# Kernel optimization log

Hardware: AMD Instinct MI355X
Metric: run time of the kernel (lower is better)

Reference implementation:

```python
import jax, jax.numpy as jnp
import numpy as np

RATIO = 4

def positional_encoding(d_model, max_len, w_s):
    # w_s: (B,) per-example frequency warp. pe[b, p, 0::2]=sin, pe[b, p, 1::2]=cos
    pos = jnp.arange(max_len, dtype=jnp.float32)                      # (L,)
    div = jnp.power(10000.0, jnp.arange(0, d_model, 2, dtype=jnp.float32) / d_model)  # (d/2,)
    ang = w_s[:, None, None] * pos[None, :, None] / div[None, None, :]  # (B, L, d/2)
    pe = jnp.stack([jnp.sin(ang), jnp.cos(ang)], axis=-1)             # (B, L, d/2, 2)
    return pe.reshape(w_s.shape[0], max_len, d_model)

def setup_inputs() -> dict:
    key = jax.random.key(0)
    ks = jax.random.split(key, 6)
    B, Tds, L, D = 32, 2048, 512, 256
    q = jax.random.normal(ks[0], (B, Tds, D), dtype=jnp.float32)
    k = jax.random.normal(ks[1], (B, L, D), dtype=jnp.float32)
    v = jax.random.normal(ks[2], (B, L, D), dtype=jnp.float32)
    w_compress = jax.random.normal(ks[3], (D // RATIO, D), dtype=jnp.float32) * (D ** -0.5)
    text_lengths = jax.random.randint(ks[4], (B,), L // 2, L + 1).at[0].set(L)
    mel_lengths = jax.random.randint(ks[5], (B,), (Tds * RATIO) // 2, Tds * RATIO + 1).at[0].set(Tds * RATIO)
    return {"q": q, "k": k, "v": v, "w_compress": w_compress,
            "text_lengths": text_lengths, "mel_lengths": mel_lengths}

def reference(q, k, v, w_compress, text_lengths, mel_lengths):
    B, Tds, D = q.shape
    L = k.shape[1]
    # padding masks (True = padded)
    text_mask = jnp.arange(L)[None, :] >= text_lengths[:, None]            # (B, L)
    mel_mask_ds = jnp.arange(Tds)[None, :] >= (mel_lengths // RATIO)[:, None]  # (B, Tds)
    # positional encodings
    q = q + positional_encoding(D, Tds, jnp.ones((B,), dtype=jnp.float32))
    w_s = mel_lengths.astype(jnp.float32) / RATIO / text_lengths.astype(jnp.float32)
    k = k + positional_encoding(D, L, w_s)
    q = q * (float(D) ** -0.5)
    # scores + masked softmax over text axis
    scores = jnp.einsum('btd,bld->btl', q, k)                              # (B, Tds, L)
    scores = jnp.where(text_mask[:, None, :], -jnp.inf, scores)
    align = jax.nn.softmax(scores, axis=-1)
    align = jnp.where(mel_mask_ds[:, :, None], 0.0, align)
    # hard argmax one-hot, straight-through blend
    idx = jnp.argmax(align, axis=-1)                                       # (B, Tds)
    align_oh = jax.nn.one_hot(idx, L, dtype=align.dtype)
    align_oh = jnp.where(mel_mask_ds[:, :, None], 0.0, align_oh)
    blend = align + jax.lax.stop_gradient(align_oh - align)
    attn = jnp.einsum('btl,bld->btd', blend, v)                            # (B, Tds, D)
    # Compress (Linear D -> D//ratio, no bias) then transpose(1,2)
    out = jnp.einsum('btd,cd->bct', attn, w_compress)                      # (B, D//ratio, Tds)
    return out, align
```

## Files before the change

### kernel.cpp

```cpp
#include <hip/hip_runtime.h>
#include <math.h>

#define NB  32
#define TDS 2048
#define LL  512
#define DD  256
#define DC  64
#define GAP_THR 4e-4f

typedef __attribute__((ext_vector_type(8)))  short short8;
typedef __attribute__((ext_vector_type(16))) float f32x16;

__device__ __forceinline__ unsigned short f2bf(float x) {
    union { float f; unsigned u; } v; v.f = x;
    unsigned r = v.u + 0x7fffu + ((v.u >> 16) & 1u);
    return (unsigned short)(r >> 16);
}
__device__ __forceinline__ float bf2f(unsigned short h) {
    union { unsigned u; float f; } v; v.u = ((unsigned)h) << 16;
    return v.f;
}
__device__ __forceinline__ void rr_sincosf(double ang, float* s, float* c) {
    double n = rint(ang * 0.15915494309189535);
    double red = fma(n, -6.283185307179586, ang);
    sincosf((float)red, s, c);
}


__global__ __launch_bounds__(256)
void tables_kernel(const float* __restrict__ k,
                   const int* __restrict__ text_lengths,
                   const int* __restrict__ mel_lengths,
                   float* __restrict__ peq,
                   char* __restrict__ kps,
                   int* __restrict__ cnt) {
    const int tid = threadIdx.x;
    if (blockIdx.x < 2048) {
        int idx = blockIdx.x * 256 + tid;
        if (idx == 0) cnt[0] = 0;
        int t = idx >> 8;
        int d = idx & 255;
        int i = d >> 1;
        double invd = exp((double)i * (-9.210340371976184 / 128.0));
        double ang = (double)t * invd;
        double s, c;
        sincos(ang, &s, &c);
        peq[idx] = (float)((d & 1) ? c : s);
        return;
    }
    __shared__ double invdiv[128];
    if (tid < 128) invdiv[tid] = exp((double)tid * (-9.210340371976184 / 128.0));
    __syncthreads();
    int f = (blockIdx.x - 2048) * 256 + tid;
    int b = f >> 14;
    int r = f & 16383;
    int ks = r >> 11;
    int r2 = r & 2047;
    int cs = r2 >> 7;
    int r3 = r2 & 127;
    int kh = r3 >> 6;
    int g  = (r3 >> 5) & 1;
    int lane32 = r3 & 31;
    int l  = cs * 32 + lane32;
    int k0 = ks * 32 + kh * 16 + g * 8;
    const float* kr = k + ((size_t)(b * LL + l)) * DD + k0;
    float4 kv0 = *(const float4*)(kr);
    float4 kv1 = *(const float4*)(kr + 4);
    float kv[8] = {kv0.x, kv0.y, kv0.z, kv0.w, kv1.x, kv1.y, kv1.z, kv1.w};
    double wsd = ((double)mel_lengths[b] * 0.25) / (double)text_lengths[b];
    double base_ang = wsd * (double)l;
    unsigned short h[8], lo8[8];
#pragma unroll
    for (int jj = 0; jj < 4; ++jj) {
        int i = (k0 >> 1) + jj;
        float sn, cs2;
        rr_sincosf(base_ang * invdiv[i], &sn, &cs2);
        float e0 = kv[2 * jj] + sn;
        float e1 = kv[2 * jj + 1] + cs2;
        h[2 * jj]       = f2bf(e0);
        h[2 * jj + 1]   = f2bf(e1);
        lo8[2 * jj]     = f2bf(e0 - bf2f(h[2 * jj]));
        lo8[2 * jj + 1] = f2bf(e1 - bf2f(h[2 * jj + 1]));
    }
    size_t off = (size_t)b * 524288 + (size_t)ks * 65536 + (size_t)cs * 4096
               + kh * 1024 + g * 512 + lane32 * 16;
    uint4 hv, lv;
    hv.x = h[0] | ((unsigned)h[1] << 16); hv.y = h[2] | ((unsigned)h[3] << 16);
    hv.z = h[4] | ((unsigned)h[5] << 16); hv.w = h[6] | ((unsigned)h[7] << 16);
    lv.x = lo8[0] | ((unsigned)lo8[1] << 16); lv.y = lo8[2] | ((unsigned)lo8[3] << 16);
    lv.z = lo8[4] | ((unsigned)lo8[5] << 16); lv.w = lo8[6] | ((unsigned)lo8[7] << 16);
    *(uint4*)(kps + off) = hv;
    *(uint4*)(kps + off + 2048) = lv;
}

__global__ __launch_bounds__(256, 3)
void score_kernel(const float* __restrict__ q,
                  const float* __restrict__ peq,
                  const char* __restrict__ kps,
                  const int* __restrict__ text_lengths,
                  const int* __restrict__ mel_lengths,
                  float* __restrict__ align_out,
                  int* __restrict__ idx_out,
                  int* __restrict__ flag_cnt,
                  int* __restrict__ flags) {
    __shared__ alignas(16) char smA[32768];
    struct Epi {
        float v1[4][32]; int i1[4][32]; float v2[4][32];
        float S[4][32];  float M[32];
    };
    __shared__ Epi ep;

    const int wgid = blockIdx.x;
    const int xcd = wgid & 7, loc = wgid >> 3;
    const int nid = xcd * 256 + loc;
    const int b  = nid >> 6;
    const int t0 = (nid & 63) << 5;

    const int tid = threadIdx.x;
    const int wn = tid >> 6, lane = tid & 63;
    const int c31 = lane & 31, hi5 = lane >> 5;
    const int tlen = text_lengths[b];
    const int melq = mel_lengths[b] >> 2;

    const char* kpb = kps + (size_t)b * 524288 + (size_t)(hi5 * 512 + c31 * 16);

    f32x16 acc[4];
#pragma unroll
    for (int ci = 0; ci < 4; ++ci)
#pragma unroll
        for (int rg = 0; rg < 16; ++rg) acc[ci][rg] = 0.f;

#define BLOAD(dst, ksv, civ)                                                    \
    {                                                                           \
        const char* p_ = kpb + (ksv) * 65536 + (wn * 4 + (civ)) * 4096;         \
        (dst)[0] = *(const short8*)(p_);                                        \
        (dst)[1] = *(const short8*)(p_ + 1024);                                 \
        (dst)[2] = *(const short8*)(p_ + 2048);                                 \
        (dst)[3] = *(const short8*)(p_ + 3072);                                 \
    }
#define MFMA6(CI, B)                                                            \
    {                                                                           \
        acc[CI] = __builtin_amdgcn_mfma_f32_32x32x16_bf16(ah0, (B)[0], acc[CI], 0, 0, 0); \
        acc[CI] = __builtin_amdgcn_mfma_f32_32x32x16_bf16(ah0, (B)[2], acc[CI], 0, 0, 0); \
        acc[CI] = __builtin_amdgcn_mfma_f32_32x32x16_bf16(al0, (B)[0], acc[CI], 0, 0, 0); \
        acc[CI] = __builtin_amdgcn_mfma_f32_32x32x16_bf16(ah1, (B)[1], acc[CI], 0, 0, 0); \
        acc[CI] = __builtin_amdgcn_mfma_f32_32x32x16_bf16(ah1, (B)[3], acc[CI], 0, 0, 0); \
        acc[CI] = __builtin_amdgcn_mfma_f32_32x32x16_bf16(al1, (B)[1], acc[CI], 0, 0, 0); \
    }

    short8 Bs[3][4];
    BLOAD(Bs[0], 0, 0)
    BLOAD(Bs[1], 0, 1)

    {
        const int sr = tid >> 3, kc = tid & 7;
        const float* qr = q   + ((size_t)(b * TDS) + t0 + sr) * DD;
        const float* pr = peq + (size_t)(t0 + sr) * DD;
#pragma unroll
        for (int kq = 0; kq < 4; ++kq) {
            int m = kq * 8 + kc;
            int k0 = m * 8;
            float4 qa = *(const float4*)(qr + k0);
            float4 qb4 = *(const float4*)(qr + k0 + 4);
            float4 pa = *(const float4*)(pr + k0);
            float4 pb = *(const float4*)(pr + k0 + 4);
            float e[8] = {(qa.x + pa.x) * 0.0625f, (qa.y + pa.y) * 0.0625f,
                          (qa.z + pa.z) * 0.0625f, (qa.w + pa.w) * 0.0625f,
                          (qb4.x + pb.x) * 0.0625f, (qb4.y + pb.y) * 0.0625f,
                          (qb4.z + pb.z) * 0.0625f, (qb4.w + pb.w) * 0.0625f};
            unsigned short h[8], lo[8];
#pragma unroll
            for (int j = 0; j < 8; ++j) {
                h[j] = f2bf(e[j]);
                lo[j] = f2bf(e[j] - bf2f(h[j]));
            }
            uint4 hv, lv;
            hv.x = h[0] | ((unsigned)h[1] << 16); hv.y = h[2] | ((unsigned)h[3] << 16);
            hv.z = h[4] | ((unsigned)h[5] << 16); hv.w = h[6] | ((unsigned)h[7] << 16);
            lv.x = lo[0] | ((unsigned)lo[1] << 16); lv.y = lo[2] | ((unsigned)lo[3] << 16);
            lv.z = lo[4] | ((unsigned)lo[5] << 16); lv.w = lo[6] | ((unsigned)lo[7] << 16);
            int base = (m >> 2) * 4096 + ((m >> 1) & 1) * 1024 + (m & 1) * 512 + sr * 16;
            *(uint4*)(smA + base) = hv;
            *(uint4*)(smA + base + 2048) = lv;
        }
    }
    __syncthreads();

    const int afr = hi5 * 512 + c31 * 16;
    short8 ah0, ah1, al0, al1;
#pragma unroll
    for (int p = 0; p < 32; ++p) {
        if ((p & 3) == 0) {
            const char* ab = smA + (p >> 2) * 4096 + afr;
            ah0 = *(const short8*)(ab);
            ah1 = *(const short8*)(ab + 1024);
            al0 = *(const short8*)(ab + 2048);
            al1 = *(const short8*)(ab + 3072);
        }
        if (p + 2 < 32) BLOAD(Bs[(p + 2) % 3], (p + 2) >> 2, (p + 2) & 3)
        MFMA6(p & 3, Bs[p % 3])
    }
#undef BLOAD
#undef MFMA6

    const float NEGINF = -__builtin_inff();
#pragma unroll
    for (int ci = 0; ci < 4; ++ci) {
        int col = wn * 128 + ci * 32 + c31;
        if (col >= tlen) {
#pragma unroll
            for (int rg = 0; rg < 16; ++rg) acc[ci][rg] = NEGINF;
        }
    }
    float v1[16]; int i1[16]; float v2[16];
#pragma unroll
    for (int rg = 0; rg < 16; ++rg) {
        v1[rg] = acc[0][rg]; i1[rg] = wn * 128 + c31; v2[rg] = NEGINF;
#pragma unroll
        for (int ci = 1; ci < 4; ++ci) {
            float v = acc[ci][rg]; int col = wn * 128 + ci * 32 + c31;
            if (v > v1[rg]) { v2[rg] = v1[rg]; v1[rg] = v; i1[rg] = col; }
            else if (v > v2[rg]) v2[rg] = v;
        }
    }
#pragma unroll
    for (int off = 1; off <= 16; off <<= 1) {
#pragma unroll
        for (int rg = 0; rg < 16; ++rg) {
            float ov1 = __shfl_xor(v1[rg], off, 64);
            int   oi1 = __shfl_xor(i1[rg], off, 64);
            float ov2 = __shfl_xor(v2[rg], off, 64);
            if (ov1 > v1[rg]) { v2[rg] = fmaxf(v1[rg], ov2); v1[rg] = ov1; i1[rg] = oi1; }
            else if (ov1 < v1[rg]) { v2[rg] = fmaxf(v2[rg], ov1); }
            else { i1[rg] = min(i1[rg], oi1); v2[rg] = v1[rg]; }
        }
    }
    if (c31 == 0) {
#pragma unroll
        for (int rg = 0; rg < 16; ++rg) {
            int r32 = (rg & 3) + 8 * (rg >> 2) + 4 * hi5;
            ep.v1[wn][r32] = v1[rg]; ep.i1[wn][r32] = i1[rg]; ep.v2[wn][r32] = v2[rg];
        }
    }
    __syncthreads();
    {
        const int r32 = c31;
        float V1 = ep.v1[0][r32]; int I1 = ep.i1[0][r32]; float V2 = ep.v2[0][r32];
#pragma unroll
        for (int w = 1; w < 4; ++w) {
            float cv1 = ep.v1[w][r32]; int ci1 = ep.i1[w][r32]; float cv2 = ep.v2[w][r32];
            if (cv1 > V1) { V2 = fmaxf(V1, cv2); V1 = cv1; I1 = ci1; }
            else if (cv1 < V1) { V2 = fmaxf(V2, cv1); }
            else { V2 = V1; }
        }
        if (wn == 0 && hi5 == 0) {
            int t = t0 + r32;
            idx_out[b * TDS + t] = I1;
            if (t < melq && (V1 - V2) < GAP_THR) {
                int pos = atomicAdd(flag_cnt, 1);
                flags[pos] = (b << 11) | t;
            }
            ep.M[r32] = V1;
        }
    }
    __syncthreads();
    float ssum[16];
#pragma unroll
    for (int rg = 0; rg < 16; ++rg) {
        int r32 = (rg & 3) + 8 * (rg >> 2) + 4 * hi5;
        float M = ep.M[r32];
        float s = 0.f;
#pragma unroll
        for (int ci = 0; ci < 4; ++ci) {
            float p = __expf(acc[ci][rg] - M);
            acc[ci][rg] = p; s += p;
        }
        ssum[rg] = s;
    }
#pragma unroll
    for (int off = 1; off <= 16; off <<= 1)
#pragma unroll
        for (int rg = 0; rg < 16; ++rg) ssum[rg] += __shfl_xor(ssum[rg], off, 64);
    if (c31 == 0) {
#pragma unroll
        for (int rg = 0; rg < 16; ++rg) {
            int r32 = (rg & 3) + 8 * (rg >> 2) + 4 * hi5;
            ep.S[wn][r32] = ssum[rg];
        }
    }
    __syncthreads();
#pragma unroll
    for (int rg = 0; rg < 16; ++rg) {
        int r32 = (rg & 3) + 8 * (rg >> 2) + 4 * hi5;
        int t = t0 + r32;
        float denom = ep.S[0][r32] + ep.S[1][r32] + ep.S[2][r32] + ep.S[3][r32];
        float sc = (t < melq) ? (1.0f / denom) : 0.f;
        size_t obase = ((size_t)(b * TDS + t)) * LL + wn * 128 + c31;
#pragma unroll
        for (int ci = 0; ci < 4; ++ci)
            __builtin_nontemporal_store(acc[ci][rg] * sc, align_out + obase + ci * 32);
    }
}

__global__ __launch_bounds__(256)
void refine_kernel(const float* __restrict__ q,
                   const float* __restrict__ k,
                   const int* __restrict__ text_lengths,
                   const int* __restrict__ mel_lengths,
                   const int* __restrict__ flags,
                   const int* __restrict__ flag_cnt,
                   int* __restrict__ idx_out) {
    __shared__ double qd[DD];
    __shared__ double invdiv[128];
    __shared__ double rbest[4];
    __shared__ int    ribest[4];
    const int tid = threadIdx.x;
    if (tid < 128)
        invdiv[tid] = 1.0 / pow(10000.0, (double)tid * (1.0 / 128.0));
    const int cnt = flag_cnt[0];
    for (int r = blockIdx.x; r < cnt; r += gridDim.x) {
        const int code = flags[r];
        const int b = code >> 11, t = code & 2047;
        const int tlen = text_lengths[b];
        const double ws = ((double)mel_lengths[b] * 0.25) / (double)text_lengths[b];
        __syncthreads();
        {
            const int d = tid, i = d >> 1;
            float sn, cs;
            rr_sincosf((double)t * invdiv[i], &sn, &cs);
            qd[d] = ((double)q[((size_t)b * TDS + t) * DD + d]
                     + (double)((d & 1) ? cs : sn)) * 0.0625;
        }
        __syncthreads();
        double best = -1.0e300; int bi = 0x7fffffff;
        for (int p = 0; p < 2; ++p) {
            const int l = tid + p * 256;
            if (l < tlen) {
                const float* kr = k + ((size_t)b * LL + l) * DD;
                const double wl = ws * (double)l;
                double sacc = 0.0;
                for (int i = 0; i < 128; ++i) {
                    float sn, cs;
                    rr_sincosf(wl * invdiv[i], &sn, &cs);
                    sacc += ((double)kr[2 * i]     + (double)sn) * qd[2 * i];
                    sacc += ((double)kr[2 * i + 1] + (double)cs) * qd[2 * i + 1];
                }
                if (sacc > best || (sacc == best && l < bi)) { best = sacc; bi = l; }
            }
        }
        for (int off = 1; off <= 32; off <<= 1) {
            double ov = __shfl_xor(best, off, 64);
            int   oi = __shfl_xor(bi, off, 64);
            if (ov > best || (ov == best && oi < bi)) { best = ov; bi = oi; }
        }
        const int wv = tid >> 6;
        if ((tid & 63) == 0) { rbest[wv] = best; ribest[wv] = bi; }
        __syncthreads();
        if (tid == 0) {
            double bb = rbest[0]; int ii = ribest[0];
            for (int w = 1; w < 4; ++w)
                if (rbest[w] > bb || (rbest[w] == bb && ribest[w] < ii)) { bb = rbest[w]; ii = ribest[w]; }
            idx_out[b * TDS + t] = ii;
        }
    }
}

__global__ __launch_bounds__(256)
void compress_kernel(const float* __restrict__ v,
                     const float* __restrict__ wc,
                     const int* __restrict__ idx_in,
                     const int* __restrict__ mel_lengths,
                     float* __restrict__ out) {
    __shared__ float Ws[16 * 68];
    __shared__ float Vs[16 * 68];
    __shared__ int   idxs[64];
    const int b   = blockIdx.y;
    const int t0  = blockIdx.x * 64;
    const int tid = threadIdx.x;
    const int melq = mel_lengths[b] >> 2;
    const float* vb = v + (size_t)b * LL * DD;

    if (tid < 64) {
        int t = t0 + tid;
        int ii = idx_in[b * TDS + t];
        idxs[tid] = (t >= melq) ? -1 : ii;
    }

    const int tx = tid >> 5;
    const int ty = tid & 31;
    const int sc = tid >> 2;
    const int su = tid & 3;
    float acc[8][2];
#pragma unroll
    for (int i = 0; i < 8; ++i) { acc[i][0] = 0.f; acc[i][1] = 0.f; }

    for (int ks = 0; ks < 16; ++ks) {
        const int d0 = ks * 16;
        __syncthreads();
        {
            float4 wv = *(const float4*)(wc + (size_t)sc * DD + d0 + su * 4);
            Ws[(su * 4 + 0) * 68 + sc] = wv.x;
            Ws[(su * 4 + 1) * 68 + sc] = wv.y;
            Ws[(su * 4 + 2) * 68 + sc] = wv.z;
            Ws[(su * 4 + 3) * 68 + sc] = wv.w;
            int row = idxs[sc];
            float4 vv = make_float4(0.f, 0.f, 0.f, 0.f);
            if (row >= 0) vv = *(const float4*)(vb + (size_t)row * DD + d0 + su * 4);
            Vs[(su * 4 + 0) * 68 + sc] = vv.x;
            Vs[(su * 4 + 1) * 68 + sc] = vv.y;
            Vs[(su * 4 + 2) * 68 + sc] = vv.z;
            Vs[(su * 4 + 3) * 68 + sc] = vv.w;
        }
        __syncthreads();
#pragma unroll
        for (int kk = 0; kk < 16; ++kk) {
            const float* wrow = Ws + kk * 68 + tx * 8;
            float4 a0 = *(const float4*)(wrow);
            float4 a1 = *(const float4*)(wrow + 4);
            float2 bb = *(const float2*)(Vs + kk * 68 + ty * 2);
            const float av[8] = {a0.x, a0.y, a0.z, a0.w, a1.x, a1.y, a1.z, a1.w};
#pragma unroll
            for (int i = 0; i < 8; ++i) {
                acc[i][0] = fmaf(av[i], bb.x, acc[i][0]);
                acc[i][1] = fmaf(av[i], bb.y, acc[i][1]);
            }
        }
    }
#pragma unroll
    for (int i = 0; i < 8; ++i) {
        int c = tx * 8 + i;
        float2 o = make_float2(acc[i][0], acc[i][1]);
        *(float2*)(out + ((size_t)(b * DC + c)) * TDS + t0 + ty * 2) = o;
    }
}

extern "C" void kernel_launch(void* const* d_in, const int* in_sizes, int n_in,
                              void* d_out, int out_size, void* d_ws, size_t ws_size,
                              hipStream_t stream) {
    const float* q    = (const float*)d_in[0];
    const float* k    = (const float*)d_in[1];
    const float* v    = (const float*)d_in[2];
    const float* wc   = (const float*)d_in[3];
    const int*   text = (const int*)d_in[4];
    const int*   mel  = (const int*)d_in[5];

    float* out   = (float*)d_out;
    float* align = out + (size_t)NB * DC * TDS;

    char*  wsb = (char*)d_ws;
    char*  KPS = wsb;
    float* PEQ = (float*)(wsb + 16777216);
    int*   IDX = (int*)(wsb + 16777216 + 2097152);
    int*   CNT = IDX + (size_t)NB * TDS;
    int*   FLG = CNT + 1;

    hipLaunchKernelGGL(tables_kernel, dim3(4096), dim3(256), 0, stream,
                       k, text, mel, PEQ, KPS, CNT);
    hipLaunchKernelGGL(score_kernel, dim3(2048), dim3(256), 0, stream,
                       q, PEQ, KPS, text, mel, align, IDX, CNT, FLG);
    hipLaunchKernelGGL(refine_kernel, dim3(256), dim3(256), 0, stream,
                       q, k, text, mel, FLG, CNT, IDX);
    hipLaunchKernelGGL(compress_kernel, dim3(TDS / 64, NB), dim3(256), 0, stream,
                       v, wc, IDX, mel, out);
}
```

Baseline: 199.5 us.

## Transpose MFMA operands so each lane owns one row, simplifying softmax epilogue

Swaps the A/B operands of the bf16 MFMAs so the accumulator is transposed: each lane now holds a single query row with 16 consecutive-ish text columns. The row-wise max/argmax/second-max and softmax sum become mostly in-register with a single cross-half shuffle, which removes the 5-stage butterfly shuffles and one block barrier. Output stores become 16-byte vector nontemporal stores instead of scalar strided stores. Tie handling in argmax now also takes the min index across waves, and correctness depends on the transposed fragment-to-column mapping being right.

```diff
diff --git a/kernel.cpp b/kernel.cpp
--- a/kernel.cpp
+++ b/kernel.cpp
@@ -10,6 +10,7 @@
 
 typedef __attribute__((ext_vector_type(8)))  short short8;
 typedef __attribute__((ext_vector_type(16))) float f32x16;
+typedef __attribute__((ext_vector_type(4)))  float f32x4;
 
 __device__ __forceinline__ unsigned short f2bf(float x) {
     union { float f; unsigned u; } v; v.f = x;
@@ -105,8 +106,7 @@
                   int* __restrict__ flags) {
     __shared__ alignas(16) char smA[32768];
     struct Epi {
-        float v1[4][32]; int i1[4][32]; float v2[4][32];
-        float S[4][32];  float M[32];
+        float v1[4][32]; int i1[4][32]; float v2[4][32]; float S[4][32];
     };
     __shared__ Epi ep;
 
@@ -140,12 +140,12 @@
     }
 #define MFMA6(CI, B)                                                            \
     {                                                                           \
-        acc[CI] = __builtin_amdgcn_mfma_f32_32x32x16_bf16(ah0, (B)[0], acc[CI], 0, 0, 0); \
-        acc[CI] = __builtin_amdgcn_mfma_f32_32x32x16_bf16(ah0, (B)[2], acc[CI], 0, 0, 0); \
-        acc[CI] = __builtin_amdgcn_mfma_f32_32x32x16_bf16(al0, (B)[0], acc[CI], 0, 0, 0); \
-        acc[CI] = __builtin_amdgcn_mfma_f32_32x32x16_bf16(ah1, (B)[1], acc[CI], 0, 0, 0); \
-        acc[CI] = __builtin_amdgcn_mfma_f32_32x32x16_bf16(ah1, (B)[3], acc[CI], 0, 0, 0); \
-        acc[CI] = __builtin_amdgcn_mfma_f32_32x32x16_bf16(al1, (B)[1], acc[CI], 0, 0, 0); \
+        acc[CI] = __builtin_amdgcn_mfma_f32_32x32x16_bf16((B)[0], ah0, acc[CI], 0, 0, 0); \
+        acc[CI] = __builtin_amdgcn_mfma_f32_32x32x16_bf16((B)[2], ah0, acc[CI], 0, 0, 0); \
+        acc[CI] = __builtin_amdgcn_mfma_f32_32x32x16_bf16((B)[0], al0, acc[CI], 0, 0, 0); \
+        acc[CI] = __builtin_amdgcn_mfma_f32_32x32x16_bf16((B)[1], ah1, acc[CI], 0, 0, 0); \
+        acc[CI] = __builtin_amdgcn_mfma_f32_32x32x16_bf16((B)[3], ah1, acc[CI], 0, 0, 0); \
+        acc[CI] = __builtin_amdgcn_mfma_f32_32x32x16_bf16((B)[1], al1, acc[CI], 0, 0, 0); \
     }
 
     short8 Bs[3][4];
@@ -204,102 +204,69 @@
 #undef MFMA6
 
     const float NEGINF = -__builtin_inff();
+    const int t = t0 + c31;
+
+    float v1 = NEGINF, v2 = NEGINF; int i1 = 0x7fffffff;
 #pragma unroll
     for (int ci = 0; ci < 4; ++ci) {
-        int col = wn * 128 + ci * 32 + c31;
-        if (col >= tlen) {
-#pragma unroll
-            for (int rg = 0; rg < 16; ++rg) acc[ci][rg] = NEGINF;
-        }
-    }
-    float v1[16]; int i1[16]; float v2[16];
-#pragma unroll
-    for (int rg = 0; rg < 16; ++rg) {
-        v1[rg] = acc[0][rg]; i1[rg] = wn * 128 + c31; v2[rg] = NEGINF;
-#pragma unroll
-        for (int ci = 1; ci < 4; ++ci) {
-            float v = acc[ci][rg]; int col = wn * 128 + ci * 32 + c31;
-            if (v > v1[rg]) { v2[rg] = v1[rg]; v1[rg] = v; i1[rg] = col; }
-            else if (v > v2[rg]) v2[rg] = v;
-        }
-    }
-#pragma unroll
-    for (int off = 1; off <= 16; off <<= 1) {
+        const int lbase = wn * 128 + ci * 32 + 4 * hi5;
 #pragma unroll
         for (int rg = 0; rg < 16; ++rg) {
-            float ov1 = __shfl_xor(v1[rg], off, 64);
-            int   oi1 = __shfl_xor(i1[rg], off, 64);
-            float ov2 = __shfl_xor(v2[rg], off, 64);
-            if (ov1 > v1[rg]) { v2[rg] = fmaxf(v1[rg], ov2); v1[rg] = ov1; i1[rg] = oi1; }
-            else if (ov1 < v1[rg]) { v2[rg] = fmaxf(v2[rg], ov1); }
-            else { i1[rg] = min(i1[rg], oi1); v2[rg] = v1[rg]; }
-        }
-    }
-    if (c31 == 0) {
+            int l = lbase + (rg & 3) + 8 * (rg >> 2);
+            float v = acc[ci][rg];
+            if (l >= tlen) { v = NEGINF; acc[ci][rg] = NEGINF; }
+            if (v > v1)      { v2 = v1; v1 = v; i1 = l; }
+            else if (v == v1) { i1 = min(i1, l); v2 = v1; }
+            else if (v > v2) { v2 = v; }
+        }
+    }
+    {
+        float ov1 = __shfl_xor(v1, 32, 64);
+        int   oi1 = __shfl_xor(i1, 32, 64);
+        float ov2 = __shfl_xor(v2, 32, 64);
+        if (ov1 > v1)      { v2 = fmaxf(v1, ov2); v1 = ov1; i1 = oi1; }
+        else if (ov1 < v1) { v2 = fmaxf(v2, ov1); }
+        else               { i1 = min(i1, oi1); v2 = v1; }
+    }
+    if (hi5 == 0) { ep.v1[wn][c31] = v1; ep.i1[wn][c31] = i1; ep.v2[wn][c31] = v2; }
+    __syncthreads();
+    float V1 = ep.v1[0][c31]; int I1 = ep.i1[0][c31]; float V2 = ep.v2[0][c31];
+#pragma unroll
+    for (int w = 1; w < 4; ++w) {
+        float cv1 = ep.v1[w][c31]; int ci1 = ep.i1[w][c31]; float cv2 = ep.v2[w][c31];
+        if (cv1 > V1)      { V2 = fmaxf(V1, cv2); V1 = cv1; I1 = ci1; }
+        else if (cv1 < V1) { V2 = fmaxf(V2, cv1); }
+        else               { I1 = min(I1, ci1); V2 = V1; }
+    }
+    if (tid < 32) {
+        idx_out[b * TDS + t] = I1;
+        if (t < melq && (V1 - V2) < GAP_THR) {
+            int pos = atomicAdd(flag_cnt, 1);
+            flags[pos] = (b << 11) | t;
+        }
+    }
+    float s = 0.f;
+#pragma unroll
+    for (int ci = 0; ci < 4; ++ci)
 #pragma unroll
         for (int rg = 0; rg < 16; ++rg) {
-            int r32 = (rg & 3) + 8 * (rg >> 2) + 4 * hi5;
-            ep.v1[wn][r32] = v1[rg]; ep.i1[wn][r32] = i1[rg]; ep.v2[wn][r32] = v2[rg];
-        }
-    }
+            float p = __expf(acc[ci][rg] - V1);
+            acc[ci][rg] = p; s += p;
+        }
+    s += __shfl_xor(s, 32, 64);
+    if (hi5 == 0) ep.S[wn][c31] = s;
     __syncthreads();
-    {
-        const int r32 = c31;
-        float V1 = ep.v1[0][r32]; int I1 = ep.i1[0][r32]; float V2 = ep.v2[0][r32];
-#pragma unroll
-        for (int w = 1; w < 4; ++w) {
-            float cv1 = ep.v1[w][r32]; int ci1 = ep.i1[w][r32]; float cv2 = ep.v2[w][r32];
-            if (cv1 > V1) { V2 = fmaxf(V1, cv2); V1 = cv1; I1 = ci1; }
-            else if (cv1 < V1) { V2 = fmaxf(V2, cv1); }
-            else { V2 = V1; }
-        }
-        if (wn == 0 && hi5 == 0) {
-            int t = t0 + r32;
-            idx_out[b * TDS + t] = I1;
-            if (t < melq && (V1 - V2) < GAP_THR) {
-                int pos = atomicAdd(flag_cnt, 1);
-                flags[pos] = (b << 11) | t;
-            }
-            ep.M[r32] = V1;
-        }
-    }
-    __syncthreads();
-    float ssum[16];
-#pragma unroll
-    for (int rg = 0; rg < 16; ++rg) {
-        int r32 = (rg & 3) + 8 * (rg >> 2) + 4 * hi5;
-        float M = ep.M[r32];
-        float s = 0.f;
-#pragma unroll
-        for (int ci = 0; ci < 4; ++ci) {
-            float p = __expf(acc[ci][rg] - M);
-            acc[ci][rg] = p; s += p;
-        }
-        ssum[rg] = s;
-    }
-#pragma unroll
-    for (int off = 1; off <= 16; off <<= 1)
-#pragma unroll
-        for (int rg = 0; rg < 16; ++rg) ssum[rg] += __shfl_xor(ssum[rg], off, 64);
-    if (c31 == 0) {
-#pragma unroll
-        for (int rg = 0; rg < 16; ++rg) {
-            int r32 = (rg & 3) + 8 * (rg >> 2) + 4 * hi5;
-            ep.S[wn][r32] = ssum[rg];
-        }
-    }
-    __syncthreads();
-#pragma unroll
-    for (int rg = 0; rg < 16; ++rg) {
-        int r32 = (rg & 3) + 8 * (rg >> 2) + 4 * hi5;
-        int t = t0 + r32;
-        float denom = ep.S[0][r32] + ep.S[1][r32] + ep.S[2][r32] + ep.S[3][r32];
-        float sc = (t < melq) ? (1.0f / denom) : 0.f;
-        size_t obase = ((size_t)(b * TDS + t)) * LL + wn * 128 + c31;
-#pragma unroll
-        for (int ci = 0; ci < 4; ++ci)
-            __builtin_nontemporal_store(acc[ci][rg] * sc, align_out + obase + ci * 32);
-    }
+    float denom = ep.S[0][c31] + ep.S[1][c31] + ep.S[2][c31] + ep.S[3][c31];
+    float sc = (t < melq) ? (1.0f / denom) : 0.f;
+    float* rowp = align_out + ((size_t)(b * TDS + t)) * LL + wn * 128 + 4 * hi5;
+#pragma unroll
+    for (int ci = 0; ci < 4; ++ci)
+#pragma unroll
+        for (int rh = 0; rh < 4; ++rh) {
+            f32x4 o = {acc[ci][rh * 4 + 0] * sc, acc[ci][rh * 4 + 1] * sc,
+                       acc[ci][rh * 4 + 2] * sc, acc[ci][rh * 4 + 3] * sc};
+            __builtin_nontemporal_store(o, (f32x4*)(rowp + ci * 32 + 8 * rh));
+        }
 }
 
 __global__ __launch_bounds__(256)
```

Measured after the change: 291.2 us. 46.0% more time.
